# Optimization experiments

Measured on AMD Instinct MI355X. Metric: run time of the kernel, lower is better.

## Reference

```python
import jax, jax.numpy as jnp
import numpy as np

N = 70
NT = 2485
M_DIM = 2000
SQ2 = float(np.sqrt(2.0))
SQH = float(np.sqrt(0.5))
_r, _c = np.tril_indices(N)
ROWS = jnp.asarray(_r)
COLS = jnp.asarray(_c)


def smat(x):
    # svec^{-1}: lower-tri fill (row-major) then symmetrize with sqrt(2) off-diag scaling
    v = jnp.reshape(x, (-1,))
    L = jnp.zeros((N, N), v.dtype).at[ROWS, COLS].set(v)
    return SQH * (L + L.T) - (SQ2 - 1.0) * L * jnp.eye(N, dtype=v.dtype)


def svec(X):
    Y = SQ2 * X - (SQ2 - 1.0) * X * jnp.eye(N, dtype=X.dtype)
    return Y[ROWS, COLS].reshape(NT, 1)


def skmult(G, K, Amat):
    # vectorized version of the per-column loop: for each column a of Amat,
    # 0.5 * svec(K smat(a) G^T + G smat(a) K^T)
    S = jax.vmap(smat, in_axes=1)(Amat)                      # [L, N, N]
    T = jnp.einsum('ij,ljk,hk->lih', K, S, G) + jnp.einsum('ij,ljk,hk->lih', G, S, K)
    return jax.vmap(svec)(0.5 * T)[:, :, 0].T                # [NT, L]


def Hp_op(U, P, Pinv):
    return 0.5 * (P @ U @ Pinv + Pinv.T @ U.T @ P.T)


def _steplen(d, Rinv, gcur):
    lam0 = jnp.linalg.eigvalsh(Rinv.T @ smat(d) @ Rinv)[0]   # smallest eigenvalue
    s = jnp.where(lam0 < 0, -1.0 / lam0, 20.0)
    return jnp.minimum(0.5, gcur * s)


def setup_inputs() -> dict:
    key = jax.random.key(0)
    ks = jax.random.split(key, 6)
    R1 = jax.random.normal(ks[0], (N, N), jnp.float32)
    X0 = R1 @ R1.T + N * jnp.eye(N, dtype=jnp.float32)
    R2 = jax.random.normal(ks[1], (N, N), jnp.float32)
    Z0 = R2 @ R2.T + N * jnp.eye(N, dtype=jnp.float32)
    x = svec(X0)
    z = svec(Z0)
    A = jax.random.normal(ks[2], (M_DIM, NT), jnp.float32) / np.float32(np.sqrt(NT))
    y = jax.random.normal(ks[3], (M_DIM, 1), jnp.float32)
    b = A @ x + 0.1 * jax.random.normal(ks[4], (M_DIM, 1), jnp.float32)
    c = z + A.T @ y + 0.1 * jax.random.normal(ks[5], (NT, 1), jnp.float32)
    normc = jnp.full((1, 1), 3.7, jnp.float32)
    return {'x': x, 'y': y, 'z': z, 'A': A, 'b': b, 'c': c, 'normc': normc}


def reference(x, y, z, A, b, c, normc):
    tol = 1e-6
    X = smat(x)
    Z = smat(z)
    Q = jnp.linalg.cholesky(X).T        # upper factor: X = Q^T Q
    P = jnp.linalg.cholesky(Z).T
    Qinv = jnp.linalg.inv(Q)
    Pinv = jnp.linalg.inv(P)
    Zinv = jnp.linalg.inv(Z)
    rp = b - A @ x
    Rd = c - z - A.T @ y
    mu = (x[:, 0] @ z[:, 0]) / 70.0
    # predictor
    Rc = -svec(Hp_op(X @ Z, P, Pinv))
    Mmat = A @ skmult(X, Zinv, A.T)
    Minv = jnp.linalg.inv(Mmat)
    h = rp + A @ (skmult(X, Zinv, Rd) - skmult(Pinv, Pinv, Rc))
    dy = Minv @ h
    dz = Rd - A.T @ dy
    dx = -x - skmult(X, Zinv, dz)
    alpha = _steplen(dx, Qinv, 0.9)
    beta = _steplen(dz, Pinv, 0.9)
    minab = jnp.minimum(alpha, beta)
    e = jnp.where((mu > tol) & (minab >= jnp.sqrt(1.0 / 3.0)),
                  jnp.maximum(1.0, 3.0 * minab * minab), 1.0)
    dot_new = (x + alpha * dx)[:, 0] @ (z + beta * dz)[:, 0]
    frac = dot_new / (x[:, 0] @ z[:, 0])
    frac_safe = jnp.where(dot_new < 0, 1.0, frac)
    sigma = jnp.where(dot_new < 0, 0.8, jnp.minimum(1.0, frac_safe ** e))
    # corrector
    Rc2 = svec(sigma * mu * jnp.eye(N, dtype=x.dtype)
               - Hp_op(X @ Z, P, Pinv)
               - Hp_op(smat(dx) @ smat(dz), P, Pinv))
    h2 = rp + A @ (skmult(X, Zinv, Rd) - skmult(Pinv, Pinv, Rc2))
    dy2 = Minv @ h2
    dz2 = Rd - A.T @ dy2
    dx2 = skmult(Pinv, Pinv, Rc2) - skmult(X, Zinv, dz2)
    g2 = 0.9 + 0.09 * minab
    alpha2 = _steplen(dx2, Qinv, g2)
    beta2 = _steplen(dz2, Pinv, g2)
    x_new = x + alpha2 * dx2
    y_new = y + beta2 * dy2
    z_new = z + beta2 * dz2
    y1 = y_new * normc
    return (x_new, y_new, z_new, y1)
```

## Files before the change

kernel.cpp:

```cpp
#include <hip/hip_runtime.h>
#include <math.h>

#define SQHf 0.70710678118654752440f

__device__ __forceinline__ void d_t2ij(int t, int& i, int& j) {
    float f = sqrtf(8.0f * (float)t + 1.0f);
    int r = (int)((f - 1.0f) * 0.5f);
    while (((r + 1) * (r + 2)) / 2 <= t) ++r;
    while ((r * (r + 1)) / 2 > t) --r;
    i = r;
    j = t - (r * (r + 1)) / 2;
}

__global__ void k_smat2(const float* __restrict__ v1, float* __restrict__ M1,
                        const float* __restrict__ v2, float* __restrict__ M2) {
    int idx = blockIdx.x * 256 + threadIdx.x;
    if (idx >= 9800) return;
    int which = idx / 4900;
    int e = idx - which * 4900;
    const float* v = which ? v2 : v1;
    float* M = which ? M2 : M1;
    int i = e / 70, j = e % 70;
    int hi = i > j ? i : j, lo = i > j ? j : i;
    float val = v[(hi * (hi + 1)) / 2 + lo];
    M[e] = (i == j) ? val : val * SQHf;
}

__global__ __launch_bounds__(256) void k_chol2(const float* __restrict__ A0, float* __restrict__ R0,
                                               const float* __restrict__ A1, float* __restrict__ R1) {
    const float* A = blockIdx.x ? A1 : A0;
    float* R = blockIdx.x ? R1 : R0;
    __shared__ float S[70][71];
    for (int e = threadIdx.x; e < 4900; e += 256) S[e / 70][e % 70] = A[e];
    __syncthreads();
    for (int k = 0; k < 70; ++k) {
        if (threadIdx.x == 0) S[k][k] = sqrtf(S[k][k]);
        __syncthreads();
        float d = S[k][k];
        for (int i = k + 1 + threadIdx.x; i < 70; i += 256) S[i][k] /= d;
        __syncthreads();
        for (int e = threadIdx.x; e < 4900; e += 256) {
            int i = e / 70, j = e % 70;
            if (j > k && i >= j) S[i][j] -= S[i][k] * S[j][k];
        }
        __syncthreads();
    }
    for (int e = threadIdx.x; e < 4900; e += 256) {
        int i = e / 70, j = e % 70;
        R[e] = (i <= j) ? S[j][i] : 0.0f;
    }
}

__global__ __launch_bounds__(256) void k_trinv2(const float* __restrict__ R0, float* __restrict__ O0,
                                                const float* __restrict__ R1, float* __restrict__ O1) {
    const float* R = blockIdx.x ? R1 : R0;
    float* O = blockIdx.x ? O1 : O0;
    __shared__ float S[70][71];
    __shared__ float V[70][71];
    for (int e = threadIdx.x; e < 4900; e += 256) S[e / 70][e % 70] = R[e];
    __syncthreads();
    int j = threadIdx.x;
    if (j < 70) {
        for (int i = j; i >= 0; --i) {
            float s = (i == j) ? 1.0f : 0.0f;
            for (int k = i + 1; k <= j; ++k) s -= S[i][k] * V[j][k];
            V[j][i] = s / S[i][i];
        }
    }
    __syncthreads();
    for (int e = threadIdx.x; e < 4900; e += 256) {
        int i = e / 70, jj = e % 70;
        O[e] = (i <= jj) ? V[jj][i] : 0.0f;
    }
}

__global__ __launch_bounds__(256) void k_mm70(const float* __restrict__ A, int tA,
                                              const float* __restrict__ B, int tB,
                                              float* __restrict__ C) {
    __shared__ float As[70][71], Bs[70][71];
    for (int e = threadIdx.x; e < 4900; e += 256) {
        int i = e / 70, j = e % 70;
        As[i][j] = tA ? A[j * 70 + i] : A[e];
        Bs[i][j] = tB ? B[j * 70 + i] : B[e];
    }
    __syncthreads();
    for (int e = threadIdx.x; e < 4900; e += 256) {
        int i = e / 70, j = e % 70;
        float s = 0.0f;
        for (int k = 0; k < 70; ++k) s += As[i][k] * Bs[k][j];
        C[e] = s;
    }
}

__global__ __launch_bounds__(256) void k_gemv_rowA(const float* __restrict__ A, long lda, int Kdim,
                                                   const float* __restrict__ v, const float* __restrict__ add,
                                                   float sgn, float* __restrict__ out) {
    int row = blockIdx.x;
    const float* Ar = A + (long)row * lda;
    float s = 0.0f;
    for (int k = threadIdx.x; k < Kdim; k += 256) s += Ar[k] * v[k];
    __shared__ float red[256];
    red[threadIdx.x] = s;
    __syncthreads();
    for (int o = 128; o; o >>= 1) {
        if (threadIdx.x < o) red[threadIdx.x] += red[threadIdx.x + o];
        __syncthreads();
    }
    if (threadIdx.x == 0) out[row] = (add ? add[row] : 0.0f) + sgn * red[0];
}

__global__ __launch_bounds__(256) void k_gemv_colAT(const float* __restrict__ A, long lda, int M, int Ncols,
                                                    const float* __restrict__ w,
                                                    const float* __restrict__ add1, const float* __restrict__ add2,
                                                    float sgn, float* __restrict__ out) {
    int j = blockIdx.x * 256 + threadIdx.x;
    if (j >= Ncols) return;
    float s = 0.0f;
    for (int i = 0; i < M; ++i) s += A[(long)i * lda + j] * w[i];
    float base = (add1 ? add1[j] : 0.0f) - (add2 ? add2[j] : 0.0f);
    out[j] = base + sgn * s;
}

__global__ __launch_bounds__(256) void k_dots_init(const float* __restrict__ x, const float* __restrict__ z,
                                                   float* __restrict__ sc) {
    __shared__ float red[256];
    float s = 0.0f;
    for (int i = threadIdx.x; i < 2485; i += 256) s += x[i] * z[i];
    red[threadIdx.x] = s;
    __syncthreads();
    for (int o = 128; o; o >>= 1) {
        if (threadIdx.x < o) red[threadIdx.x] += red[threadIdx.x + o];
        __syncthreads();
    }
    if (threadIdx.x == 0) { sc[1] = red[0]; sc[0] = red[0] / 70.0f; }
}

__global__ __launch_bounds__(256) void k_dot_new(const float* __restrict__ x, const float* __restrict__ dx,
                                                 const float* __restrict__ z, const float* __restrict__ dz,
                                                 float* __restrict__ sc) {
    __shared__ float red[256];
    float a = sc[2], b = sc[3];
    float s = 0.0f;
    for (int i = threadIdx.x; i < 2485; i += 256)
        s += (x[i] + a * dx[i]) * (z[i] + b * dz[i]);
    red[threadIdx.x] = s;
    __syncthreads();
    for (int o = 128; o; o >>= 1) {
        if (threadIdx.x < o) red[threadIdx.x] += red[threadIdx.x + o];
        __syncthreads();
    }
    if (threadIdx.x == 0) sc[7] = red[0];
}

__global__ __launch_bounds__(256) void k_rc_chain(const float* __restrict__ X, const float* __restrict__ Z,
                                                  const float* __restrict__ Pu, const float* __restrict__ Pi,
                                                  float* __restrict__ W1out, float* __restrict__ Rc) {
    __shared__ float A[70][71], B[70][71], C[70][71];
    int tid = threadIdx.x;
    for (int e = tid; e < 4900; e += 256) { A[e / 70][e % 70] = X[e]; B[e / 70][e % 70] = Z[e]; }
    __syncthreads();
    for (int e = tid; e < 4900; e += 256) {
        int i = e / 70, j = e % 70;
        float s = 0.0f;
        for (int k = 0; k < 70; ++k) s += A[i][k] * B[k][j];
        C[i][j] = s;
    }
    __syncthreads();
    for (int e = tid; e < 4900; e += 256) A[e / 70][e % 70] = Pu[e];
    __syncthreads();
    for (int e = tid; e < 4900; e += 256) {
        int i = e / 70, j = e % 70;
        float s = 0.0f;
        for (int k = 0; k < 70; ++k) s += A[i][k] * C[k][j];
        B[i][j] = s;
    }
    __syncthreads();
    for (int e = tid; e < 4900; e += 256) A[e / 70][e % 70] = Pi[e];
    __syncthreads();
    for (int e = tid; e < 4900; e += 256) {
        int i = e / 70, j = e % 70;
        float s = 0.0f;
        for (int k = 0; k < 70; ++k) s += B[i][k] * A[k][j];
        C[i][j] = s;
        W1out[e] = s;
    }
    __syncthreads();
    for (int t = tid; t < 2485; t += 256) {
        int i, j;
        d_t2ij(t, i, j);
        float v = (i == j) ? C[i][i] : (C[i][j] + C[j][i]) * SQHf;
        Rc[t] = -v;
    }
}

__global__ __launch_bounds__(256) void k_rc2_chain(const float* __restrict__ dxv, const float* __restrict__ dzv,
                                                   const float* __restrict__ Pu, const float* __restrict__ Pi,
                                                   const float* __restrict__ W1, const float* __restrict__ sc,
                                                   float* __restrict__ Rc2) {
    __shared__ float A[70][71], B[70][71], C[70][71];
    int tid = threadIdx.x;
    for (int e = tid; e < 4900; e += 256) {
        int i = e / 70, j = e % 70;
        int hi = i > j ? i : j, lo = i > j ? j : i;
        float vx = dxv[(hi * (hi + 1)) / 2 + lo];
        float vz = dzv[(hi * (hi + 1)) / 2 + lo];
        A[i][j] = (i == j) ? vx : vx * SQHf;
        B[i][j] = (i == j) ? vz : vz * SQHf;
    }
    __syncthreads();
    for (int e = tid; e < 4900; e += 256) {
        int i = e / 70, j = e % 70;
        float s = 0.0f;
        for (int k = 0; k < 70; ++k) s += A[i][k] * B[k][j];
        C[i][j] = s;
    }
    __syncthreads();
    for (int e = tid; e < 4900; e += 256) A[e / 70][e % 70] = Pu[e];
    __syncthreads();
    for (int e = tid; e < 4900; e += 256) {
        int i = e / 70, j = e % 70;
        float s = 0.0f;
        for (int k = 0; k < 70; ++k) s += A[i][k] * C[k][j];
        B[i][j] = s;
    }
    __syncthreads();
    for (int e = tid; e < 4900; e += 256) A[e / 70][e % 70] = Pi[e];
    __syncthreads();
    for (int e = tid; e < 4900; e += 256) {
        int i = e / 70, j = e % 70;
        float s = 0.0f;
        for (int k = 0; k < 70; ++k) s += B[i][k] * A[k][j];
        C[i][j] = s;
    }
    __syncthreads();
    float sm = sc[13];
    for (int t = tid; t < 2485; t += 256) {
        int i, j;
        d_t2ij(t, i, j);
        if (i == j)
            Rc2[t] = sm - W1[i * 70 + i] - C[i][i];
        else
            Rc2[t] = -(W1[i * 70 + j] + W1[j * 70 + i] + C[i][j] + C[j][i]) * SQHf;
    }
}

__global__ __launch_bounds__(256) void k_skmult(const float* __restrict__ K, const float* __restrict__ G,
                                                const float* __restrict__ Arows, long ldA,
                                                float* __restrict__ outT, long ldOut) {
    int l = blockIdx.x;
    const float* a = Arows + (long)l * ldA;
    float* out = outT + (long)l * ldOut;
    __shared__ float S[70][71];
    __shared__ float T1[70][71];
    for (int e = threadIdx.x; e < 4900; e += 256) {
        int i = e / 70, j = e % 70;
        int hi = i > j ? i : j, lo = i > j ? j : i;
        float v = a[(hi * (hi + 1)) / 2 + lo];
        S[i][j] = (i == j) ? v : v * SQHf;
    }
    __syncthreads();
    for (int e = threadIdx.x; e < 4900; e += 256) {
        int i = e / 70, j = e % 70;
        const float* Gr = G + j * 70;
        float s = 0.0f;
        for (int k = 0; k < 70; ++k) s += S[i][k] * Gr[k];
        T1[i][j] = s;
    }
    __syncthreads();
    for (int t = threadIdx.x; t < 2485; t += 256) {
        int i, j;
        d_t2ij(t, i, j);
        const float* Ki = K + i * 70;
        const float* Kj = K + j * 70;
        float wij = 0.0f, wji = 0.0f;
        for (int k = 0; k < 70; ++k) {
            wij += Ki[k] * T1[k][j];
            wji += Kj[k] * T1[k][i];
        }
        out[t] = (i == j) ? wij : (wij + wji) * SQHf;
    }
}

#define GBM 64
#define GBK 32
__global__ __launch_bounds__(256) void k_gemm_nt(const float* __restrict__ A, long lda,
                                                 const float* __restrict__ B, long ldb,
                                                 float* __restrict__ C, long ldc,
                                                 int M, int N, int Kd,
                                                 float alpha, float beta, int lower_only) {
    int bx = blockIdx.x, by = blockIdx.y;
    int row0 = by * GBM, col0 = bx * GBM;
    if (lower_only && col0 > row0 + GBM - 1) return;
    __shared__ float As[GBM][GBK + 1], Bs[GBM][GBK + 1];
    int tid = threadIdx.x;
    int tx = tid % 16, ty = tid / 16;
    float acc[4][4] = {{0.f}};
    for (int k0 = 0; k0 < Kd; k0 += GBK) {
        for (int e = tid; e < GBM * GBK; e += 256) {
            int r = e / GBK, cc = e % GBK;
            int gr = row0 + r, gc = k0 + cc;
            As[r][cc] = (gr < M && gc < Kd) ? A[(long)gr * lda + gc] : 0.0f;
        }
        for (int e = tid; e < GBM * GBK; e += 256) {
            int r = e / GBK, cc = e % GBK;
            int gr = col0 + r, gc = k0 + cc;
            Bs[r][cc] = (gr < N && gc < Kd) ? B[(long)gr * ldb + gc] : 0.0f;
        }
        __syncthreads();
        for (int kk = 0; kk < GBK; ++kk) {
            float av[4], bv[4];
#pragma unroll
            for (int m = 0; m < 4; ++m) av[m] = As[ty * 4 + m][kk];
#pragma unroll
            for (int n = 0; n < 4; ++n) bv[n] = Bs[tx * 4 + n][kk];
#pragma unroll
            for (int m = 0; m < 4; ++m)
#pragma unroll
                for (int n = 0; n < 4; ++n) acc[m][n] += av[m] * bv[n];
        }
        __syncthreads();
    }
#pragma unroll
    for (int m = 0; m < 4; ++m)
#pragma unroll
        for (int n = 0; n < 4; ++n) {
            int gr = row0 + ty * 4 + m, gc = col0 + tx * 4 + n;
            if (gr < M && gc < N) {
                float* cp = &C[(long)gr * ldc + gc];
                if (beta != 0.0f) *cp = beta * (*cp) + alpha * acc[m][n];
                else *cp = alpha * acc[m][n];
            }
        }
}

__global__ __launch_bounds__(256) void k_chol_diag_inv(float* __restrict__ Mp, long ld, int jb, int nb,
                                                       float* __restrict__ Linv) {
    __shared__ float S[64][65];
    __shared__ float V[64][65];
    int tid = threadIdx.x;
    for (int e = tid; e < nb * nb; e += 256) S[e / nb][e % nb] = Mp[(long)(jb + e / nb) * ld + jb + e % nb];
    __syncthreads();
    for (int k = 0; k < nb; ++k) {
        if (tid == 0) S[k][k] = sqrtf(S[k][k]);
        __syncthreads();
        float d = S[k][k];
        for (int i = k + 1 + tid; i < nb; i += 256) S[i][k] /= d;
        __syncthreads();
        for (int e = tid; e < nb * nb; e += 256) {
            int i = e / nb, j = e % nb;
            if (j > k && i >= j) S[i][j] -= S[i][k] * S[j][k];
        }
        __syncthreads();
    }
    for (int e = tid; e < nb * nb; e += 256) {
        int i = e / nb, j = e % nb;
        if (i >= j) Mp[(long)(jb + i) * ld + jb + j] = S[i][j];
    }
    if (tid < nb) {
        int c = tid;
        V[c][c] = 1.0f / S[c][c];
        for (int i = c + 1; i < nb; ++i) {
            float s = 0.0f;
            for (int k = c; k < i; ++k) s += S[i][k] * V[k][c];
            V[i][c] = -s / S[i][i];
        }
    }
    __syncthreads();
    for (int e = tid; e < 4096; e += 256) {
        int i = e >> 6, j = e & 63;
        Linv[e] = (i < nb && j < nb && i >= j) ? V[i][j] : 0.0f;
    }
}

__global__ __launch_bounds__(256) void k_panel_trsm(float* __restrict__ Mp, long ld, int jb, int nb, int n,
                                                    const float* __restrict__ Linv) {
    __shared__ float Vs[64][65];
    __shared__ float As[64][65];
    int r0 = jb + nb + blockIdx.x * 64;
    int nrows = n - r0;
    if (nrows > 64) nrows = 64;
    if (nrows <= 0) return;
    int tid = threadIdx.x;
    for (int e = tid; e < 4096; e += 256) { int i = e >> 6, j = e & 63; Vs[i][j] = Linv[e]; }
    for (int e = tid; e < nrows * nb; e += 256) {
        int i = e / nb, j = e % nb;
        As[i][j] = Mp[(long)(r0 + i) * ld + jb + j];
    }
    __syncthreads();
    int tx = tid % 16, ty = tid / 16;
    float acc[4][4] = {{0.f}};
    for (int k = 0; k < nb; ++k) {
        float av[4], bv[4];
#pragma unroll
        for (int m = 0; m < 4; ++m) av[m] = As[ty * 4 + m][k];
#pragma unroll
        for (int c = 0; c < 4; ++c) bv[c] = Vs[tx * 4 + c][k];
#pragma unroll
        for (int m = 0; m < 4; ++m)
#pragma unroll
            for (int c = 0; c < 4; ++c) acc[m][c] += av[m] * bv[c];
    }
#pragma unroll
    for (int m = 0; m < 4; ++m)
#pragma unroll
        for (int c = 0; c < 4; ++c) {
            int gr = ty * 4 + m, gc = tx * 4 + c;
            if (gr < nrows && gc < nb) Mp[(long)(r0 + gr) * ld + jb + gc] = acc[m][c];
        }
}

__global__ __launch_bounds__(1024) void k_spdsolve2(const float* __restrict__ L, long ld, int n,
                                                    const float* __restrict__ Linv,
                                                    const float* __restrict__ bin, float* __restrict__ xout) {
    __shared__ float bv[2048];
    __shared__ float yt[64];
    int tid = threadIdx.x;
    for (int i = tid; i < n; i += 1024) bv[i] = bin[i];
    __syncthreads();
    int nblk = (n + 63) / 64;
    int r = tid >> 4, l = tid & 15;
    for (int t = 0; t < nblk; ++t) {
        int jb = t * 64;
        int nb = n - jb < 64 ? n - jb : 64;
        const float* Vi = Linv + (long)t * 4096;
        float s = 0.0f;
        if (r < nb) {
            for (int c = l; c < nb; c += 16) s += Vi[r * 64 + c] * bv[jb + c];
        }
        s += __shfl_down(s, 8, 16);
        s += __shfl_down(s, 4, 16);
        s += __shfl_down(s, 2, 16);
        s += __shfl_down(s, 1, 16);
        if (l == 0 && r < 64) yt[r] = s;
        __syncthreads();
        for (int i = tid; i < nb; i += 1024) bv[jb + i] = yt[i];
        __syncthreads();
        for (int i = jb + nb + tid; i < n; i += 1024) {
            const float* Lr = L + (long)i * ld + jb;
            float acc = 0.0f;
            if (nb == 64) {
                const float4* L4 = (const float4*)Lr;
#pragma unroll
                for (int m = 0; m < 16; ++m) {
                    float4 q = L4[m];
                    acc += q.x * bv[jb + 4 * m] + q.y * bv[jb + 4 * m + 1] + q.z * bv[jb + 4 * m + 2] + q.w * bv[jb + 4 * m + 3];
                }
            } else {
                for (int m = 0; m < nb; ++m) acc += Lr[m] * bv[jb + m];
            }
            bv[i] -= acc;
        }
        __syncthreads();
    }
    for (int t = nblk - 1; t >= 0; --t) {
        int jb = t * 64;
        int nb = n - jb < 64 ? n - jb : 64;
        const float* Vi = Linv + (long)t * 4096;
        float s = 0.0f;
        if (r < nb) {
            for (int c = l; c < nb; c += 16) s += Vi[c * 64 + r] * bv[jb + c];
        }
        s += __shfl_down(s, 8, 16);
        s += __shfl_down(s, 4, 16);
        s += __shfl_down(s, 2, 16);
        s += __shfl_down(s, 1, 16);
        if (l == 0 && r < 64) yt[r] = s;
        __syncthreads();
        for (int i = tid; i < nb; i += 1024) bv[jb + i] = yt[i];
        __syncthreads();
        for (int i = tid; i < jb; i += 1024) {
            float acc = 0.0f;
            for (int m = 0; m < nb; ++m) acc += L[(long)(jb + m) * ld + i] * bv[jb + m];
            bv[i] -= acc;
        }
        __syncthreads();
    }
    for (int i = tid; i < n; i += 1024) xout[i] = bv[i];
}

__device__ __forceinline__ int jac_f(int i, int r) {
    return (i == 0) ? 0 : 1 + ((i - 1 + r) % 69);
}
__global__ __launch_bounds__(256) void k_steplen_eig(const float* __restrict__ dxv, const float* __restrict__ dzv,
                                                     const float* __restrict__ Qi, const float* __restrict__ Pi,
                                                     float* __restrict__ sc, int o0, int o1) {
    const float* v = blockIdx.x ? dzv : dxv;
    const float* Rm = blockIdx.x ? Pi : Qi;
    int outi = blockIdx.x ? o1 : o0;
    __shared__ float S[70][71], T[70][71], A[70][71];
    __shared__ float cs[35], sn[35];
    int tid = threadIdx.x;
    for (int e = tid; e < 4900; e += 256) {
        int i = e / 70, j = e % 70;
        int hi = i > j ? i : j, lo = i > j ? j : i;
        float val = v[(hi * (hi + 1)) / 2 + lo];
        S[i][j] = (i == j) ? val : val * SQHf;
        A[i][j] = Rm[e];
    }
    __syncthreads();
    for (int e = tid; e < 4900; e += 256) {
        int i = e / 70, j = e % 70;
        float s = 0.0f;
        for (int k = 0; k < 70; ++k) s += A[k][i] * S[k][j];
        T[i][j] = s;
    }
    __syncthreads();
    for (int e = tid; e < 4900; e += 256) {
        int i = e / 70, j = e % 70;
        float s = 0.0f;
        for (int k = 0; k < 70; ++k) s += T[i][k] * A[k][j];
        S[i][j] = s;
    }
    __syncthreads();
    for (int sw = 0; sw < 6; ++sw) {
        for (int rr = 0; rr < 69; ++rr) {
            if (tid < 35) {
                int p = jac_f(tid, rr), q = jac_f(69 - tid, rr);
                float app = S[p][p], aqq = S[q][q], apq = S[p][q];
                float cc = 1.0f, ss = 0.0f;
                float denom = fabsf(app) + fabsf(aqq);
                if (fabsf(apq) > 1e-12f * denom + 1e-30f) {
                    float tau = (aqq - app) / (2.0f * apq);
                    float t = ((tau >= 0.0f) ? 1.0f : -1.0f) / (fabsf(tau) + sqrtf(1.0f + tau * tau));
                    cc = 1.0f / sqrtf(1.0f + t * t);
                    ss = t * cc;
                }
                cs[tid] = cc;
                sn[tid] = ss;
            }
            __syncthreads();
            for (int t = tid; t < 1225; t += 256) {
                int a = t / 35, b = t - a * 35;
                int pa = jac_f(a, rr), qa = jac_f(69 - a, rr);
                int pb = jac_f(b, rr), qb = jac_f(69 - b, rr);
                float ca = cs[a], sa = sn[a], cb = cs[b], sb = sn[b];
                float m00 = S[pa][pb], m01 = S[pa][qb], m10 = S[qa][pb], m11 = S[qa][qb];
                float r00 = ca * m00 - sa * m10, r01 = ca * m01 - sa * m11;
                float r10 = sa * m00 + ca * m10, r11 = sa * m01 + ca * m11;
                S[pa][pb] = cb * r00 - sb * r01;
                S[pa][qb] = sb * r00 + cb * r01;
                S[qa][pb] = cb * r10 - sb * r11;
                S[qa][qb] = sb * r10 + cb * r11;
            }
            __syncthreads();
        }
    }
    __shared__ float red[256];
    float mn = 1e30f;
    for (int i = tid; i < 70; i += 256) mn = fminf(mn, S[i][i]);
    red[tid] = mn;
    __syncthreads();
    for (int o = 128; o; o >>= 1) {
        if (tid < o) red[tid] = fminf(red[tid], red[tid + o]);
        __syncthreads();
    }
    if (tid == 0) sc[outi] = red[0];
}

__global__ void k_pred_scalars(float* sc) {
    float l0a = sc[11], l0b = sc[12];
    float sa = (l0a < 0.0f) ? -1.0f / l0a : 20.0f;
    float sb = (l0b < 0.0f) ? -1.0f / l0b : 20.0f;
    float alpha = fminf(0.5f, 0.9f * sa);
    float beta = fminf(0.5f, 0.9f * sb);
    float minab = fminf(alpha, beta);
    sc[2] = alpha;
    sc[3] = beta;
    sc[4] = minab;
    float mu = sc[0];
    sc[5] = (mu > 1e-6f && minab >= 0.57735026918962576f) ? fmaxf(1.0f, 3.0f * minab * minab) : 1.0f;
}
__global__ void k_sigma(float* sc) {
    float dn = sc[7], xz = sc[1], e = sc[5];
    float frac = dn / xz;
    float fs = (dn < 0.0f) ? 1.0f : frac;
    float sig = (dn < 0.0f) ? 0.8f : fminf(1.0f, powf(fs, e));
    sc[6] = sig;
    sc[13] = sig * sc[0];
    sc[8] = 0.9f + 0.09f * sc[4];
}
__global__ void k_corr_scalars(float* sc) {
    float g2 = sc[8];
    float l0a = sc[14], l0b = sc[15];
    float sa = (l0a < 0.0f) ? -1.0f / l0a : 20.0f;
    float sb = (l0b < 0.0f) ? -1.0f / l0b : 20.0f;
    sc[9] = fminf(0.5f, g2 * sa);
    sc[10] = fminf(0.5f, g2 * sb);
}

__global__ void k_axpby(const float* __restrict__ u, const float* __restrict__ v,
                        float a, float b, float* __restrict__ out, int n) {
    int i = blockIdx.x * 256 + threadIdx.x;
    if (i < n) out[i] = a * u[i] + b * v[i];
}

__global__ void k_final(const float* __restrict__ x, const float* __restrict__ y, const float* __restrict__ z,
                        const float* __restrict__ dx2, const float* __restrict__ dy2, const float* __restrict__ dz2,
                        const float* __restrict__ normc, const float* __restrict__ sc, float* __restrict__ out) {
    int i = blockIdx.x * 256 + threadIdx.x;
    float a2 = sc[9], b2 = sc[10];
    if (i < 2485) out[i] = x[i] + a2 * dx2[i];
    else if (i < 4485) { int j = i - 2485; out[i] = y[j] + b2 * dy2[j]; }
    else if (i < 6970) { int j = i - 4485; out[i] = z[j] + b2 * dz2[j]; }
    else if (i < 8970) { int j = i - 6970; out[i] = (y[j] + b2 * dy2[j]) * normc[0]; }
}

extern "C" void kernel_launch(void* const* d_in, const int* in_sizes, int n_in,
                              void* d_out, int out_size, void* d_ws, size_t ws_size,
                              hipStream_t stream) {
    const float* x = (const float*)d_in[0];
    const float* y = (const float*)d_in[1];
    const float* z = (const float*)d_in[2];
    const float* A = (const float*)d_in[3];
    const float* b = (const float*)d_in[4];
    const float* c = (const float*)d_in[5];
    const float* normc = (const float*)d_in[6];
    float* out = (float*)d_out;
    float* ws = (float*)d_ws;

    float* SKT = ws;
    float* Mm = ws + 4970000;
    float* S0 = ws + 8970000;
    float* X = S0;
    float* Z = S0 + 4900;
    float* Qu = S0 + 9800;
    float* Pu = S0 + 14700;
    float* Qi = S0 + 19600;
    float* Pi = S0 + 24500;
    float* Zi = S0 + 29400;
    float* W1 = S0 + 44100;
    float* rp = S0 + 83300;
    float* h = S0 + 85300;
    float* dy = S0 + 87300;
    float* dy2 = S0 + 89300;
    float* h2 = S0 + 91300;
    float* Rd = S0 + 93300;
    float* Rc = S0 + 95785;
    float* k1 = S0 + 98270;
    float* k2 = S0 + 100755;
    float* dz = S0 + 103240;
    float* dx = S0 + 105725;
    float* Rc2 = S0 + 108210;
    float* k2b = S0 + 110695;
    float* dz2 = S0 + 113180;
    float* dx2 = S0 + 115665;
    float* tmpv = S0 + 118150;
    float* sc = S0 + 120635;
    float* Linv = S0 + 121000;

    k_smat2<<<39, 256, 0, stream>>>(x, X, z, Z);
    k_chol2<<<2, 256, 0, stream>>>(X, Qu, Z, Pu);
    k_trinv2<<<2, 256, 0, stream>>>(Qu, Qi, Pu, Pi);
    k_mm70<<<1, 256, 0, stream>>>(Pi, 0, Pi, 1, Zi);

    k_gemv_rowA<<<2000, 256, 0, stream>>>(A, 2485L, 2485, x, b, -1.0f, rp);
    k_gemv_colAT<<<10, 256, 0, stream>>>(A, 2485L, 2000, 2485, y, c, z, -1.0f, Rd);
    k_dots_init<<<1, 256, 0, stream>>>(x, z, sc);

    k_rc_chain<<<1, 256, 0, stream>>>(X, Z, Pu, Pi, W1, Rc);

    k_skmult<<<2000, 256, 0, stream>>>(X, Zi, A, 2485L, SKT, 2485L);
    k_gemm_nt<<<dim3(32, 32), 256, 0, stream>>>(A, 2485L, SKT, 2485L, Mm, 2000L,
                                                2000, 2000, 2485, 1.0f, 0.0f, 1);

    for (int jb = 0; jb < 2000; jb += 64) {
        int nb = (2000 - jb) < 64 ? (2000 - jb) : 64;
        float* Lslot = Linv + (long)(jb / 64) * 4096;
        k_chol_diag_inv<<<1, 256, 0, stream>>>(Mm, 2000L, jb, nb, Lslot);
        int rows = 2000 - jb - nb;
        if (rows > 0) {
            int gb = (rows + 63) / 64;
            k_panel_trsm<<<gb, 256, 0, stream>>>(Mm, 2000L, jb, nb, 2000, Lslot);
            const float* pan = Mm + (size_t)(jb + nb) * 2000 + jb;
            float* csub = Mm + (size_t)(jb + nb) * 2000 + (jb + nb);
            k_gemm_nt<<<dim3(gb, gb), 256, 0, stream>>>(pan, 2000L, pan, 2000L, csub, 2000L,
                                                        rows, rows, nb, -1.0f, 1.0f, 1);
        }
    }

    k_skmult<<<1, 256, 0, stream>>>(X, Zi, Rd, 0L, k1, 0L);
    k_skmult<<<1, 256, 0, stream>>>(Pi, Pi, Rc, 0L, k2, 0L);
    k_axpby<<<10, 256, 0, stream>>>(k1, k2, 1.0f, -1.0f, tmpv, 2485);
    k_gemv_rowA<<<2000, 256, 0, stream>>>(A, 2485L, 2485, tmpv, rp, 1.0f, h);
    k_spdsolve2<<<1, 1024, 0, stream>>>(Mm, 2000L, 2000, Linv, h, dy);
    k_gemv_colAT<<<10, 256, 0, stream>>>(A, 2485L, 2000, 2485, dy, Rd, (const float*)0, -1.0f, dz);
    k_skmult<<<1, 256, 0, stream>>>(X, Zi, dz, 0L, tmpv, 0L);
    k_axpby<<<10, 256, 0, stream>>>(x, tmpv, -1.0f, -1.0f, dx, 2485);

    k_steplen_eig<<<2, 256, 0, stream>>>(dx, dz, Qi, Pi, sc, 11, 12);
    k_pred_scalars<<<1, 1, 0, stream>>>(sc);
    k_dot_new<<<1, 256, 0, stream>>>(x, dx, z, dz, sc);
    k_sigma<<<1, 1, 0, stream>>>(sc);

    k_rc2_chain<<<1, 256, 0, stream>>>(dx, dz, Pu, Pi, W1, sc, Rc2);
    k_skmult<<<1, 256, 0, stream>>>(Pi, Pi, Rc2, 0L, k2b, 0L);
    k_axpby<<<10, 256, 0, stream>>>(k1, k2b, 1.0f, -1.0f, tmpv, 2485);
    k_gemv_rowA<<<2000, 256, 0, stream>>>(A, 2485L, 2485, tmpv, rp, 1.0f, h2);
    k_spdsolve2<<<1, 1024, 0, stream>>>(Mm, 2000L, 2000, Linv, h2, dy2);
    k_gemv_colAT<<<10, 256, 0, stream>>>(A, 2485L, 2000, 2485, dy2, Rd, (const float*)0, -1.0f, dz2);
    k_skmult<<<1, 256, 0, stream>>>(X, Zi, dz2, 0L, tmpv, 0L);
    k_axpby<<<10, 256, 0, stream>>>(k2b, tmpv, 1.0f, -1.0f, dx2, 2485);

    k_steplen_eig<<<2, 256, 0, stream>>>(dx2, dz2, Qi, Pi, sc, 14, 15);
    k_corr_scalars<<<1, 1, 0, stream>>>(sc);

    k_final<<<36, 256, 0, stream>>>(x, y, z, dx2, dy2, dz2, normc, sc, out);
}
```

Before: 12.68 ms.

## Invert Cholesky factor explicitly and replace serial triangular solves with parallel matvecs

Replaces the single-block forward/back substitution with an explicit inverse of the lower Cholesky factor, built by recursive doubling of block-triangular GEMMs starting from the existing 64x64 diagonal-block inverses. The two solves then become a lower-triangular matvec and a transposed matvec split across many blocks. The A^T gemv is also split over row chunks with a separate reduction pass so more blocks run at once. This adds O(n^3) inversion work and more kernel launches, in exchange for removing the serial single-workgroup solves that occupied one compute unit.

```diff
diff --git a/kernel.cpp b/kernel.cpp
--- a/kernel.cpp
+++ b/kernel.cpp
@@ -2,6 +2,8 @@
 #include <math.h>
 
 #define SQHf 0.70710678118654752440f
+
+struct Pairs16 { int4 q[16]; };
 
 __device__ __forceinline__ void d_t2ij(int t, int& i, int& j) {
     float f = sqrtf(8.0f * (float)t + 1.0f);
@@ -109,14 +111,24 @@
     if (threadIdx.x == 0) out[row] = (add ? add[row] : 0.0f) + sgn * red[0];
 }
 
-__global__ __launch_bounds__(256) void k_gemv_colAT(const float* __restrict__ A, long lda, int M, int Ncols,
-                                                    const float* __restrict__ w,
-                                                    const float* __restrict__ add1, const float* __restrict__ add2,
-                                                    float sgn, float* __restrict__ out) {
+__global__ __launch_bounds__(256) void k_colAT_part(const float* __restrict__ A, long lda, int M, int Ncols,
+                                                    const float* __restrict__ w, float* __restrict__ partial) {
+    int j = blockIdx.x * 256 + threadIdx.x;
+    int s = blockIdx.y;
+    int rpb = (M + gridDim.y - 1) / gridDim.y;
+    int i0 = s * rpb, i1 = i0 + rpb < M ? i0 + rpb : M;
+    float acc = 0.0f;
+    if (j < Ncols)
+        for (int i = i0; i < i1; ++i) acc += A[(long)i * lda + j] * w[i];
+    if (j < Ncols) partial[(long)s * Ncols + j] = acc;
+}
+__global__ __launch_bounds__(256) void k_colAT_fin(const float* __restrict__ partial, int S, int Ncols,
+                                                   const float* __restrict__ add1, const float* __restrict__ add2,
+                                                   float sgn, float* __restrict__ out) {
     int j = blockIdx.x * 256 + threadIdx.x;
     if (j >= Ncols) return;
     float s = 0.0f;
-    for (int i = 0; i < M; ++i) s += A[(long)i * lda + j] * w[i];
+    for (int k = 0; k < S; ++k) s += partial[(long)k * Ncols + j];
     float base = (add1 ? add1[j] : 0.0f) - (add2 ? add2[j] : 0.0f);
     out[j] = base + sgn * s;
 }
@@ -333,6 +345,127 @@
         }
 }
 
+__device__ __forceinline__ void gemm_nn_dev(const float* __restrict__ A, long lda,
+                                            const float* __restrict__ B, long ldb,
+                                            float* __restrict__ C, long ldc,
+                                            int M, int N, int K, float alpha) {
+    int row0 = blockIdx.y * 64, col0 = blockIdx.x * 64;
+    if (row0 >= M || col0 >= N) return;
+    __shared__ float As[64][33], Bs[32][65];
+    int tid = threadIdx.x;
+    int tx = tid % 16, ty = tid / 16;
+    float acc[4][4] = {{0.f}};
+    for (int k0 = 0; k0 < K; k0 += 32) {
+        for (int e = tid; e < 64 * 32; e += 256) {
+            int r = e / 32, cc = e % 32;
+            As[r][cc] = (row0 + r < M && k0 + cc < K) ? A[(long)(row0 + r) * lda + k0 + cc] : 0.0f;
+        }
+        for (int e = tid; e < 32 * 64; e += 256) {
+            int kk = e / 64, nn = e % 64;
+            Bs[kk][nn] = (k0 + kk < K && col0 + nn < N) ? B[(long)(k0 + kk) * ldb + col0 + nn] : 0.0f;
+        }
+        __syncthreads();
+        for (int kk = 0; kk < 32; ++kk) {
+            float av[4], bv[4];
+#pragma unroll
+            for (int m = 0; m < 4; ++m) av[m] = As[ty * 4 + m][kk];
+#pragma unroll
+            for (int n = 0; n < 4; ++n) bv[n] = Bs[kk][tx * 4 + n];
+#pragma unroll
+            for (int m = 0; m < 4; ++m)
+#pragma unroll
+                for (int n = 0; n < 4; ++n) acc[m][n] += av[m] * bv[n];
+        }
+        __syncthreads();
+    }
+#pragma unroll
+    for (int m = 0; m < 4; ++m)
+#pragma unroll
+        for (int n = 0; n < 4; ++n) {
+            int gr = row0 + ty * 4 + m, gc = col0 + tx * 4 + n;
+            if (gr < M && gc < N) C[(long)gr * ldc + gc] = alpha * acc[m][n];
+        }
+}
+
+__global__ __launch_bounds__(256) void k_tri_phaseA(const float* __restrict__ Mm, long ld,
+                                                    float* __restrict__ tmp, Pairs16 pl, int np) {
+    int z = blockIdx.z;
+    if (z >= np) return;
+    int p0 = pl.q[z].x, h = pl.q[z].y, n = pl.q[z].z, toff = pl.q[z].w;
+    gemm_nn_dev(Mm + (long)(p0 + h) * ld + p0, ld,
+                Mm + (long)p0 * ld + p0, ld,
+                tmp + toff, h, n - h, h, h, 1.0f);
+}
+__global__ __launch_bounds__(256) void k_tri_phaseB(float* __restrict__ Mm, long ld,
+                                                    const float* __restrict__ tmp, Pairs16 pl, int np) {
+    int z = blockIdx.z;
+    if (z >= np) return;
+    int p0 = pl.q[z].x, h = pl.q[z].y, n = pl.q[z].z, toff = pl.q[z].w;
+    int M = n - h;
+    gemm_nn_dev(Mm + (long)(p0 + h) * ld + (p0 + h), ld,
+                tmp + toff, h,
+                Mm + (long)(p0 + h) * ld + p0, ld, M, h, M, -1.0f);
+}
+
+__global__ void k_zero_upper(float* __restrict__ Mm, int n) {
+    int row0 = blockIdx.y * 64, col0 = blockIdx.x * 64;
+    if (col0 <= row0) return;
+    for (int e = threadIdx.x; e < 4096; e += 256) {
+        int i = row0 + (e >> 6), j = col0 + (e & 63);
+        if (i < n && j < n) Mm[(long)i * n + j] = 0.0f;
+    }
+}
+
+__global__ void k_copy_diaginv(float* __restrict__ Mm, long ld, int n, const float* __restrict__ Linv) {
+    int t = blockIdx.x;
+    int jb = t * 64;
+    int nb = n - jb < 64 ? n - jb : 64;
+    if (nb <= 0) return;
+    const float* Vi = Linv + (long)t * 4096;
+    for (int e = threadIdx.x; e < nb * nb; e += 256) {
+        int i = e / nb, j = e % nb;
+        Mm[(long)(jb + i) * ld + jb + j] = Vi[i * 64 + j];
+    }
+}
+
+__global__ __launch_bounds__(256) void k_trimv_low(const float* __restrict__ W, long ld, int n,
+                                                   const float* __restrict__ h, float* __restrict__ out) {
+    int i = blockIdx.x;
+    const float* Wr = W + (long)i * ld;
+    float s = 0.0f;
+    for (int k = threadIdx.x; k <= i; k += 256) s += Wr[k] * h[k];
+    __shared__ float red[256];
+    red[threadIdx.x] = s;
+    __syncthreads();
+    for (int o = 128; o; o >>= 1) {
+        if (threadIdx.x < o) red[threadIdx.x] += red[threadIdx.x + o];
+        __syncthreads();
+    }
+    if (threadIdx.x == 0) out[i] = red[0];
+}
+
+__global__ __launch_bounds__(256) void k_trimvT_part(const float* __restrict__ W, long ld, int n,
+                                                     const float* __restrict__ v, float* __restrict__ partial) {
+    int j = blockIdx.x * 256 + threadIdx.x;
+    int s = blockIdx.y;
+    int rpb = (n + gridDim.y - 1) / gridDim.y;
+    int i0 = s * rpb, i1 = i0 + rpb < n ? i0 + rpb : n;
+    float acc = 0.0f;
+    if (j < n) {
+        int ist = i0 > j ? i0 : j;
+        for (int i = ist; i < i1; ++i) acc += W[(long)i * ld + j] * v[i];
+        partial[(long)s * n + j] = acc;
+    }
+}
+__global__ __launch_bounds__(256) void k_part_reduce(const float* __restrict__ partial, int S, int n,
+                                                     float* __restrict__ out) {
+    int j = blockIdx.x * 256 + threadIdx.x;
+    if (j >= n) return;
+    float s = 0.0f;
+    for (int k = 0; k < S; ++k) s += partial[(long)k * n + j];
+    out[j] = s;
+}
+
 __global__ __launch_bounds__(256) void k_chol_diag_inv(float* __restrict__ Mp, long ld, int jb, int nb,
                                                        float* __restrict__ Linv) {
     __shared__ float S[64][65];
@@ -407,75 +540,6 @@
             int gr = ty * 4 + m, gc = tx * 4 + c;
             if (gr < nrows && gc < nb) Mp[(long)(r0 + gr) * ld + jb + gc] = acc[m][c];
         }
-}
-
-__global__ __launch_bounds__(1024) void k_spdsolve2(const float* __restrict__ L, long ld, int n,
-                                                    const float* __restrict__ Linv,
-                                                    const float* __restrict__ bin, float* __restrict__ xout) {
-    __shared__ float bv[2048];
-    __shared__ float yt[64];
-    int tid = threadIdx.x;
-    for (int i = tid; i < n; i += 1024) bv[i] = bin[i];
-    __syncthreads();
-    int nblk = (n + 63) / 64;
-    int r = tid >> 4, l = tid & 15;
-    for (int t = 0; t < nblk; ++t) {
-        int jb = t * 64;
-        int nb = n - jb < 64 ? n - jb : 64;
-        const float* Vi = Linv + (long)t * 4096;
-        float s = 0.0f;
-        if (r < nb) {
-            for (int c = l; c < nb; c += 16) s += Vi[r * 64 + c] * bv[jb + c];
-        }
-        s += __shfl_down(s, 8, 16);
-        s += __shfl_down(s, 4, 16);
-        s += __shfl_down(s, 2, 16);
-        s += __shfl_down(s, 1, 16);
-        if (l == 0 && r < 64) yt[r] = s;
-        __syncthreads();
-        for (int i = tid; i < nb; i += 1024) bv[jb + i] = yt[i];
-        __syncthreads();
-        for (int i = jb + nb + tid; i < n; i += 1024) {
-            const float* Lr = L + (long)i * ld + jb;
-            float acc = 0.0f;
-            if (nb == 64) {
-                const float4* L4 = (const float4*)Lr;
-#pragma unroll
-                for (int m = 0; m < 16; ++m) {
-                    float4 q = L4[m];
-                    acc += q.x * bv[jb + 4 * m] + q.y * bv[jb + 4 * m + 1] + q.z * bv[jb + 4 * m + 2] + q.w * bv[jb + 4 * m + 3];
-                }
-            } else {
-                for (int m = 0; m < nb; ++m) acc += Lr[m] * bv[jb + m];
-            }
-            bv[i] -= acc;
-        }
-        __syncthreads();
-    }
-    for (int t = nblk - 1; t >= 0; --t) {
-        int jb = t * 64;
-        int nb = n - jb < 64 ? n - jb : 64;
-        const float* Vi = Linv + (long)t * 4096;
-        float s = 0.0f;
-        if (r < nb) {
-            for (int c = l; c < nb; c += 16) s += Vi[c * 64 + r] * bv[jb + c];
-        }
-        s += __shfl_down(s, 8, 16);
-        s += __shfl_down(s, 4, 16);
-        s += __shfl_down(s, 2, 16);
-        s += __shfl_down(s, 1, 16);
-        if (l == 0 && r < 64) yt[r] = s;
-        __syncthreads();
-        for (int i = tid; i < nb; i += 1024) bv[jb + i] = yt[i];
-        __syncthreads();
-        for (int i = tid; i < jb; i += 1024) {
-            float acc = 0.0f;
-            for (int m = 0; m < nb; ++m) acc += L[(long)(jb + m) * ld + i] * bv[jb + m];
-            bv[i] -= acc;
-        }
-        __syncthreads();
-    }
-    for (int i = tid; i < n; i += 1024) xout[i] = bv[i];
 }
 
 __device__ __forceinline__ int jac_f(int i, int r) {
@@ -647,6 +711,8 @@
     float* tmpv = S0 + 118150;
     float* sc = S0 + 120635;
     float* Linv = S0 + 121000;
+    float* v1 = S0 + 253000;
+    float* pbuf = S0 + 256000;
 
     k_smat2<<<39, 256, 0, stream>>>(x, X, z, Z);
     k_chol2<<<2, 256, 0, stream>>>(X, Qu, Z, Pu);
@@ -654,7 +720,8 @@
     k_mm70<<<1, 256, 0, stream>>>(Pi, 0, Pi, 1, Zi);
 
     k_gemv_rowA<<<2000, 256, 0, stream>>>(A, 2485L, 2485, x, b, -1.0f, rp);
-    k_gemv_colAT<<<10, 256, 0, stream>>>(A, 2485L, 2000, 2485, y, c, z, -1.0f, Rd);
+    k_colAT_part<<<dim3(10, 16), 256, 0, stream>>>(A, 2485L, 2000, 2485, y, pbuf);
+    k_colAT_fin<<<10, 256, 0, stream>>>(pbuf, 16, 2485, c, z, -1.0f, Rd);
     k_dots_init<<<1, 256, 0, stream>>>(x, z, sc);
 
     k_rc_chain<<<1, 256, 0, stream>>>(X, Z, Pu, Pi, W1, Rc);
@@ -678,12 +745,34 @@
         }
     }
 
+    k_zero_upper<<<dim3(32, 32), 256, 0, stream>>>(Mm, 2000);
+    k_copy_diaginv<<<32, 256, 0, stream>>>(Mm, 2000L, 2000, Linv);
+    for (int bs = 64; bs < 2000; bs *= 2) {
+        Pairs16 pl;
+        int np = 0, maxM = 0, toff = 0;
+        for (int p0 = 0; p0 + bs < 2000; p0 += 2 * bs) {
+            int hh = bs;
+            int nn = (2 * bs < 2000 - p0) ? 2 * bs : (2000 - p0);
+            pl.q[np].x = p0; pl.q[np].y = hh; pl.q[np].z = nn; pl.q[np].w = toff;
+            toff += (nn - hh) * hh;
+            if (nn - hh > maxM) maxM = nn - hh;
+            ++np;
+        }
+        if (np == 0) continue;
+        dim3 g((bs + 63) / 64, (maxM + 63) / 64, np);
+        k_tri_phaseA<<<g, 256, 0, stream>>>(Mm, 2000L, SKT, pl, np);
+        k_tri_phaseB<<<g, 256, 0, stream>>>(Mm, 2000L, SKT, pl, np);
+    }
+
     k_skmult<<<1, 256, 0, stream>>>(X, Zi, Rd, 0L, k1, 0L);
     k_skmult<<<1, 256, 0, stream>>>(Pi, Pi, Rc, 0L, k2, 0L);
     k_axpby<<<10, 256, 0, stream>>>(k1, k2, 1.0f, -1.0f, tmpv, 2485);
     k_gemv_rowA<<<2000, 256, 0, stream>>>(A, 2485L, 2485, tmpv, rp, 1.0f, h);
-    k_spdsolve2<<<1, 1024, 0, stream>>>(Mm, 2000L, 2000, Linv, h, dy);
-    k_gemv_colAT<<<10, 256, 0, stream>>>(A, 2485L, 2000, 2485, dy, Rd, (const float*)0, -1.0f, dz);
+    k_trimv_low<<<2000, 256, 0, stream>>>(Mm, 2000L, 2000, h, v1);
+    k_trimvT_part<<<dim3(8, 16), 256, 0, stream>>>(Mm, 2000L, 2000, v1, pbuf);
+    k_part_reduce<<<8, 256, 0, stream>>>(pbuf, 16, 2000, dy);
+    k_colAT_part<<<dim3(10, 16), 256, 0, stream>>>(A, 2485L, 2000, 2485, dy, pbuf);
+    k_colAT_fin<<<10, 256, 0, stream>>>(pbuf, 16, 2485, Rd, (const float*)0, -1.0f, dz);
     k_skmult<<<1, 256, 0, stream>>>(X, Zi, dz, 0L, tmpv, 0L);
     k_axpby<<<10, 256, 0, stream>>>(x, tmpv, -1.0f, -1.0f, dx, 2485);
 
@@ -696,8 +785,11 @@
     k_skmult<<<1, 256, 0, stream>>>(Pi, Pi, Rc2, 0L, k2b, 0L);
     k_axpby<<<10, 256, 0, stream>>>(k1, k2b, 1.0f, -1.0f, tmpv, 2485);
     k_gemv_rowA<<<2000, 256, 0, stream>>>(A, 2485L, 2485, tmpv, rp, 1.0f, h2);
-    k_spdsolve2<<<1, 1024, 0, stream>>>(Mm, 2000L, 2000, Linv, h2, dy2);
-    k_gemv_colAT<<<10, 256, 0, stream>>>(A, 2485L, 2000, 2485, dy2, Rd, (const float*)0, -1.0f, dz2);
+    k_trimv_low<<<2000, 256, 0, stream>>>(Mm, 2000L, 2000, h2, v1);
+    k_trimvT_part<<<dim3(8, 16), 256, 0, stream>>>(Mm, 2000L, 2000, v1, pbuf);
+    k_part_reduce<<<8, 256, 0, stream>>>(pbuf, 16, 2000, dy2);
+    k_colAT_part<<<dim3(10, 16), 256, 0, stream>>>(A, 2485L, 2000, 2485, dy2, pbuf);
+    k_colAT_fin<<<10, 256, 0, stream>>>(pbuf, 16, 2485, Rd, (const float*)0, -1.0f, dz2);
     k_skmult<<<1, 256, 0, stream>>>(X, Zi, dz2, 0L, tmpv, 0L);
     k_axpby<<<10, 256, 0, stream>>>(k2b, tmpv, 1.0f, -1.0f, dx2, 2485);
 
```

Result: faster. 10.31 ms (-18.7%).
